# Kernel optimization log

Measured on AMD Instinct MI355X. Metric: run time of the kernel, lower is better.

## Reference

```python
import jax, jax.numpy as jnp
import numpy as np

B, S, H, NH, HD = 2, 2048, 4096, 32, 128
THETA = 10000.0


def rotate_half(x):
    x1, x2 = jnp.split(x, 2, axis=-1)
    return jnp.concatenate((-x2, x1), axis=-1)


def setup_inputs() -> dict:
    key = jax.random.key(0)
    ks = jax.random.split(key, 6)
    hidden_states = jax.random.normal(ks[0], (B, S, H), dtype=jnp.float32)
    # additive causal mask, [1,1,S,S]
    causal = jnp.triu(jnp.full((S, S), -1e9, dtype=jnp.float32), k=1)
    attention_mask = causal[None, None, :, :]
    scale = 0.02
    Wq = jax.random.normal(ks[1], (H, H), dtype=jnp.float32) * scale
    Wk = jax.random.normal(ks[2], (H, H), dtype=jnp.float32) * scale
    Wv = jax.random.normal(ks[3], (H, H), dtype=jnp.float32) * scale
    Wo = jax.random.normal(ks[4], (H, H), dtype=jnp.float32) * scale
    return {"hidden_states": hidden_states, "attention_mask": attention_mask,
            "Wq": Wq, "Wk": Wk, "Wv": Wv, "Wo": Wo}


def _rope_tables(seq_len, dtype):
    inv_freq = 1.0 / (THETA ** (jnp.arange(0, HD, 2, dtype=jnp.float32) / HD))
    t = jnp.arange(seq_len, dtype=jnp.float32)
    freqs = jnp.einsum('i,j->ij', t, inv_freq)          # [S, HD/2]
    emb = jnp.concatenate((freqs, freqs), axis=-1)       # [S, HD]
    return jnp.cos(emb).astype(dtype), jnp.sin(emb).astype(dtype)


def reference(hidden_states, attention_mask, Wq, Wk, Wv, Wo):
    b, s, _ = hidden_states.shape
    # nn.Linear: y = x @ W.T
    q = jnp.einsum('bsh,oh->bso', hidden_states, Wq).reshape(b, s, NH, HD).transpose(0, 2, 1, 3)
    k = jnp.einsum('bsh,oh->bso', hidden_states, Wk).reshape(b, s, NH, HD).transpose(0, 2, 1, 3)
    v = jnp.einsum('bsh,oh->bso', hidden_states, Wv).reshape(b, s, NH, HD).transpose(0, 2, 1, 3)
    cos, sin = _rope_tables(s, q.dtype)                  # [S, HD] broadcast over b,h
    q = q * cos + rotate_half(q) * sin
    k = k * cos + rotate_half(k) * sin
    scores = jnp.einsum('bhqd,bhkd->bhqk', q, k) / jnp.sqrt(jnp.asarray(HD, q.dtype))
    scores = scores + attention_mask
    attn = jax.nn.softmax(scores.astype(jnp.float32), axis=-1).astype(q.dtype)
    out = jnp.einsum('bhqk,bhkd->bhqd', attn, v)
    out = out.transpose(0, 2, 1, 3).reshape(b, s, H)
    return jnp.einsum('bsh,oh->bso', out, Wo)
```

## Files before the change

kernel.cpp:

```cpp
#include <hip/hip_runtime.h>
#include <stdint.h>

typedef __attribute__((ext_vector_type(4))) float f32x4;
typedef __attribute__((ext_vector_type(8))) short bf16x8;
typedef __attribute__((ext_vector_type(4))) unsigned int u32x4;

__device__ __forceinline__ short f2bf(float x) {
  unsigned int u = __builtin_bit_cast(unsigned int, x);
  unsigned int r = (u + 0x7fffu + ((u >> 16) & 1u)) >> 16;
  return (short)r;
}
__device__ __forceinline__ float bf2f(short s) {
  unsigned int u = ((unsigned int)(unsigned short)s) << 16;
  return __builtin_bit_cast(float, u);
}
__device__ __forceinline__ unsigned pkbf(float lo, float hi) {
  unsigned r;
  asm("v_cvt_pk_bf16_f32 %0, %1, %2" : "=v"(r) : "v"(lo), "v"(hi));
  return r;
}

__device__ __forceinline__ void gload_lds16(const void* g, void* l) {
  __builtin_amdgcn_global_load_lds(
      (const __attribute__((address_space(1))) void*)g,
      (__attribute__((address_space(3))) void*)l, 16, 0, 0);
}

__global__ __launch_bounds__(256) void cvt5(const float* __restrict__ a,
                                            const float* __restrict__ b,
                                            const float* __restrict__ c,
                                            const float* __restrict__ d,
                                            const float* __restrict__ e,
                                            short* __restrict__ oa,
                                            short* __restrict__ ob,
                                            short* __restrict__ oc,
                                            short* __restrict__ od,
                                            short* __restrict__ oe, int n) {
  int y = blockIdx.y;
  const float* in = (y == 0) ? a : (y == 1) ? b : (y == 2) ? c : (y == 3) ? d : e;
  short* out = (y == 0) ? oa : (y == 1) ? ob : (y == 2) ? oc : (y == 3) ? od : oe;
  int idx = blockIdx.x * blockDim.x + threadIdx.x;
  int stride = gridDim.x * blockDim.x;
  for (int i = idx * 4; i < n; i += stride * 4) {
    float4 v = *(const float4*)(in + i);
    short4 o;
    o.x = f2bf(v.x); o.y = f2bf(v.y); o.z = f2bf(v.z); o.w = f2bf(v.w);
    *(short4*)(out + i) = o;
  }
}

__global__ __launch_bounds__(256) void cvt_bf16(const float* __restrict__ in,
                                                short* __restrict__ out, int n) {
  int idx = blockIdx.x * blockDim.x + threadIdx.x;
  int stride = gridDim.x * blockDim.x;
  for (int i = idx * 4; i < n; i += stride * 4) {
    float4 v = *(const float4*)(in + i);
    short4 o;
    o.x = f2bf(v.x); o.y = f2bf(v.y); o.z = f2bf(v.z); o.w = f2bf(v.w);
    *(short4*)(out + i) = o;
  }
}

__global__ __launch_bounds__(256) void rope_table_k(float2* __restrict__ tab) {
  int idx = blockIdx.x * 256 + threadIdx.x;
  int s = idx >> 6, j = idx & 63;
  float invf = powf(10000.0f, -((float)j) / 64.0f);
  float a = (float)s * invf;
  tab[idx] = make_float2(cosf(a), sinf(a));
}

__global__ __launch_bounds__(256) void rope_apply_k(short* __restrict__ Qb,
                                                    short* __restrict__ Kb,
                                                    const float2* __restrict__ tab) {
  bool isK = (blockIdx.y != 0);
  short* base = isK ? Kb : Qb;
  float post = isK ? 1.0f : (0.08838834764831845f * 1.4426950408889634f);
  int token = blockIdx.x;
  int s = token & 2047;
  short* rowp = base + (size_t)token * 4096;
  const float2* trow = tab + s * 64;
  for (int u = threadIdx.x; u < 512; u += 256) {
    int h = u >> 4;
    int d0 = (u & 15) * 4;
    short* p1 = rowp + h * 128 + d0;
    short* p2 = p1 + 64;
    short4 a = *(short4*)p1, b = *(short4*)p2;
    short4 ra, rb;
#pragma unroll
    for (int j = 0; j < 4; ++j) {
      short aj = (&a.x)[j], bj = (&b.x)[j];
      float qa = bf2f(aj), qb = bf2f(bj);
      float2 cs = trow[d0 + j];
      (&ra.x)[j] = f2bf((qa * cs.x - qb * cs.y) * post);
      (&rb.x)[j] = f2bf((qb * cs.x + qa * cs.y) * post);
    }
    *(short4*)p1 = ra;
    *(short4*)p2 = rb;
  }
}

template <int MODE>
__global__ __launch_bounds__(512) void gemm8p(const short* __restrict__ A,
                                              const short* __restrict__ Bw,
                                              void* __restrict__ out) {
  __shared__ __attribute__((aligned(16))) short smem[2 * 32768];
  int wg = blockIdx.x;
  int xcd = wg & 7, ii = wg >> 3;
  int by = xcd * 2 + (ii >> 4);
  int bx = ii & 15;
  int tid = threadIdx.x;
  int w = tid >> 6, lane = tid & 63;
  int l16 = lane & 15, l4 = lane >> 4;
  int wm = w >> 2, wn = w & 3;

  f32x4 acc[8][4] = {};

  const short* Ab = A + (size_t)(by * 256) * 4096;
  const short* Bb = Bw + (size_t)(bx * 256) * 4096;

  auto STAGE_MAT = [&](int kt, int isB) {
    const short* src = isB ? Bb : Ab;
    int ob = (kt & 1) * 32768 + isB * 16384;
#pragma unroll
    for (int j = 0; j < 4; ++j) {
      int c = j * 512 + tid;
      int row = c >> 3;
      int sc = (c & 7) ^ (row & 7);
      gload_lds16(src + (size_t)row * 4096 + kt * 64 + sc * 8, &smem[ob + c * 8]);
    }
  };

  bf16x8 bfr[4];
  auto PHASE = [&](int ob, int kk, int mh, bool loadB) {
    const short* lA = &smem[ob];
    const short* lB = &smem[ob + 16384];
    if (loadB) {
#pragma unroll
      for (int nf = 0; nf < 4; ++nf) {
        int row = wn * 64 + nf * 16 + l16;
        int phys = (kk * 4 + l4) ^ (row & 7);
        bfr[nf] = *(const bf16x8*)&lB[row * 64 + phys * 8];
      }
    }
    bf16x8 af[4];
#pragma unroll
    for (int mf = 0; mf < 4; ++mf) {
      int row = wm * 128 + mh * 64 + mf * 16 + l16;
      int phys = (kk * 4 + l4) ^ (row & 7);
      af[mf] = *(const bf16x8*)&lA[row * 64 + phys * 8];
    }
    __builtin_amdgcn_s_setprio(1);
#pragma unroll
    for (int mf = 0; mf < 4; ++mf)
#pragma unroll
      for (int nf = 0; nf < 4; ++nf)
        acc[mh * 4 + mf][nf] =
            __builtin_amdgcn_mfma_f32_16x16x32_bf16(af[mf], bfr[nf], acc[mh * 4 + mf][nf], 0, 0, 0);
    __builtin_amdgcn_s_setprio(0);
    __builtin_amdgcn_s_barrier();
    asm volatile("" ::: "memory");
  };

  STAGE_MAT(0, 0);
  STAGE_MAT(0, 1);
  asm volatile("s_waitcnt vmcnt(0)" ::: "memory");
  __builtin_amdgcn_s_barrier();
  asm volatile("" ::: "memory");

  const int b0 = 0, b1 = 32768;
  for (int i = 0; i < 32; ++i) {
    int kt1 = 2 * i + 1;
    STAGE_MAT(kt1, 0);
    asm volatile("s_waitcnt vmcnt(4)" ::: "memory");
    __builtin_amdgcn_s_barrier();
    asm volatile("" ::: "memory");
    PHASE(b0, 0, 0, true);
    STAGE_MAT(kt1, 1);
    PHASE(b0, 0, 1, false);
    PHASE(b0, 1, 0, true);
    PHASE(b0, 1, 1, false);
    if (i + 1 < 32) {
      STAGE_MAT(2 * i + 2, 0);
      asm volatile("s_waitcnt vmcnt(4)" ::: "memory");
    } else {
      asm volatile("s_waitcnt vmcnt(0)" ::: "memory");
    }
    __builtin_amdgcn_s_barrier();
    asm volatile("" ::: "memory");
    PHASE(b1, 0, 0, true);
    if (i + 1 < 32) STAGE_MAT(2 * i + 2, 1);
    PHASE(b1, 0, 1, false);
    PHASE(b1, 1, 0, true);
    PHASE(b1, 1, 1, false);
  }

  int orow0 = by * 256 + wm * 128;
  int ocol0 = bx * 256 + wn * 64;
#pragma unroll
  for (int mf = 0; mf < 8; ++mf)
#pragma unroll
    for (int nf = 0; nf < 4; ++nf)
#pragma unroll
      for (int k = 0; k < 4; ++k) {
        int r = orow0 + mf * 16 + l4 * 4 + k;
        int c = ocol0 + nf * 16 + l16;
        float v = acc[mf][nf][k];
        if constexpr (MODE == 0) {
          ((short*)out)[(size_t)r * 4096 + c] = f2bf(v);
        } else if constexpr (MODE == 1) {
          ((float*)out)[(size_t)r * 4096 + c] = v;
        } else {
          int bb = r >> 11, ss = r & 2047;
          int h = c >> 7, d = c & 127;
          ((short*)out)[(((size_t)((bb * 32 + h) * 128 + d)) << 11) + ss] = f2bf(v);
        }
      }
}

__global__ __launch_bounds__(512, 4) void attn_k(const short* __restrict__ Qb,
                                                 const short* __restrict__ Kb,
                                                 const short* __restrict__ Vt,
                                                 short* __restrict__ AO) {
  __shared__ __attribute__((aligned(16))) short smem[24576];
  int p = blockIdx.x;
  int bh = p & 63;
  int qt = 15 - (p >> 6);
  int b = bh >> 5, h = bh & 31;
  int tid = threadIdx.x, w = tid >> 6, lane = tid & 63;
  int l16 = lane & 15, l4 = lane >> 4;

  const int nt = 2 * qt + 2;
  const int qbase = qt * 128 + w * 16;

  bf16x8 qf[4];
  {
    const short* Qg = Qb + (size_t)(b * 2048 + qbase + l16) * 4096 + h * 128 + l4 * 8;
#pragma unroll
    for (int kk = 0; kk < 4; ++kk) qf[kk] = *(const bf16x8*)(Qg + kk * 32);
  }

  f32x4 oacc[8] = {};
  float mrun = -1e30f, lsum = 0.f;

  const short* Kbase = Kb + (size_t)(b * 2048) * 4096 + h * 128;
  const short* Vbase = Vt + (size_t)bh * 128 * 2048;

  auto STAGE_K = [&](int t, int sel) {
    short* lK = &smem[sel * 8192];
#pragma unroll
    for (int j = 0; j < 2; ++j) {
      int c = j * 512 + tid;
      int row = c >> 4;
      int src = (c & 15) ^ (row & 15);
      gload_lds16(Kbase + (size_t)(t * 64 + row) * 4096 + src * 8, &lK[c * 8]);
    }
  };
  auto STAGE_V = [&](int t) {
    short* lV = &smem[16384];
#pragma unroll
    for (int j = 0; j < 2; ++j) {
      int c = j * 512 + tid;
      int row = c >> 3;
      int src = (c & 7) ^ (row & 7);
      gload_lds16(Vbase + (size_t)row * 2048 + t * 64 + src * 8, &lV[c * 8]);
    }
  };

  STAGE_V(0);
  STAGE_K(0, 0);
  STAGE_K(1, 1);

  const int src0 = l16 | ((2 * (l4 & 1)) << 4);
  const int src1 = src0 | 16;
  const bool hiA = (l4 >> 1) != 0;

  for (int t = 0; t < nt; ++t) {
    if (t == nt - 1)
      asm volatile("s_waitcnt vmcnt(0)" ::: "memory");
    else
      asm volatile("s_waitcnt vmcnt(2)" ::: "memory");
    __builtin_amdgcn_s_barrier();
    asm volatile("" ::: "memory");

    bool skip = (t * 64 > qbase + 15);
    if (!skip) {
      const short* lK = &smem[(t & 1) * 8192];
      const short* lV = &smem[16384];

      f32x4 sacc[4] = {};
#pragma unroll
      for (int kk = 0; kk < 4; ++kk) {
#pragma unroll
        for (int n4 = 0; n4 < 4; ++n4) {
          int row = n4 * 16 + l16;
          int phys = (kk * 4 + l4) ^ (row & 15);
          bf16x8 kf = *(const bf16x8*)&lK[row * 128 + phys * 8];
          sacc[n4] = __builtin_amdgcn_mfma_f32_16x16x32_bf16(kf, qf[kk], sacc[n4], 0, 0, 0);
        }
      }

      if (t * 64 + 63 > qbase) {
        int q = qbase + l16;
#pragma unroll
        for (int n4 = 0; n4 < 4; ++n4)
#pragma unroll
          for (int i = 0; i < 4; ++i) {
            int kv = t * 64 + n4 * 16 + l4 * 4 + i;
            if (kv > q) sacc[n4][i] = -1e30f;
          }
      }

      {
        float v0 = fmaxf(fmaxf(sacc[0][0], sacc[0][1]), fmaxf(sacc[0][2], sacc[0][3]));
        float v1 = fmaxf(fmaxf(sacc[1][0], sacc[1][1]), fmaxf(sacc[1][2], sacc[1][3]));
        float v2 = fmaxf(fmaxf(sacc[2][0], sacc[2][1]), fmaxf(sacc[2][2], sacc[2][3]));
        float v3 = fmaxf(fmaxf(sacc[3][0], sacc[3][1]), fmaxf(sacc[3][2], sacc[3][3]));
        float vm = fmaxf(fmaxf(v0, v1), fmaxf(v2, v3));
        vm = fmaxf(vm, __shfl_xor(vm, 16));
        vm = fmaxf(vm, __shfl_xor(vm, 32));
        if (!__all(vm - mrun <= 8.0f)) {
          float mnew = fmaxf(mrun, vm);
          float fsc = __builtin_amdgcn_exp2f(mrun - mnew);
          mrun = mnew;
          lsum *= fsc;
#pragma unroll
          for (int dg = 0; dg < 8; ++dg) oacc[dg] *= fsc;
        }
        float psum = 0.f;
#pragma unroll
        for (int n4 = 0; n4 < 4; ++n4)
#pragma unroll
          for (int i = 0; i < 4; ++i) {
            float e = __builtin_amdgcn_exp2f(sacc[n4][i] - mrun);
            sacc[n4][i] = e;
            psum += e;
          }
        psum += __shfl_xor(psum, 16);
        psum += __shfl_xor(psum, 32);
        lsum += psum;
      }

#pragma unroll
      for (int c = 0; c < 2; ++c) {
        unsigned pk0h0 = pkbf(sacc[2 * c][0], sacc[2 * c][1]);
        unsigned pk0h1 = pkbf(sacc[2 * c][2], sacc[2 * c][3]);
        unsigned pk1h0 = pkbf(sacc[2 * c + 1][0], sacc[2 * c + 1][1]);
        unsigned pk1h1 = pkbf(sacc[2 * c + 1][2], sacc[2 * c + 1][3]);
        unsigned s00 = __shfl((int)pk0h0, src0), s10 = __shfl((int)pk1h0, src0);
        unsigned s01 = __shfl((int)pk0h1, src0), s11 = __shfl((int)pk1h1, src0);
        unsigned t00 = __shfl((int)pk0h0, src1), t10 = __shfl((int)pk1h0, src1);
        unsigned t01 = __shfl((int)pk0h1, src1), t11 = __shfl((int)pk1h1, src1);
        u32x4 uw;
        uw[0] = hiA ? s10 : s00;
        uw[1] = hiA ? s11 : s01;
        uw[2] = hiA ? t10 : t00;
        uw[3] = hiA ? t11 : t01;
        bf16x8 pb = __builtin_bit_cast(bf16x8, uw);
#pragma unroll
        for (int dg = 0; dg < 8; ++dg) {
          int d = dg * 16 + l16;
          int phys = (c * 4 + l4) ^ (l16 & 7);
          bf16x8 vf = *(const bf16x8*)&lV[d * 64 + phys * 8];
          oacc[dg] = __builtin_amdgcn_mfma_f32_16x16x32_bf16(vf, pb, oacc[dg], 0, 0, 0);
        }
      }
    }

    __builtin_amdgcn_s_barrier();
    asm volatile("" ::: "memory");
    if (t + 1 < nt) STAGE_V(t + 1);
    if (t + 2 < nt) STAGE_K(t + 2, t & 1);
  }

  __syncthreads();
  short* reg = &smem[w * 2048];
  float rls = 1.0f / lsum;
#pragma unroll
  for (int dg = 0; dg < 8; ++dg) {
    unsigned u0 = pkbf(oacc[dg][0] * rls, oacc[dg][1] * rls);
    unsigned u1 = pkbf(oacc[dg][2] * rls, oacc[dg][3] * rls);
    int cc = dg * 2 + (l4 >> 1);
    int phys = cc ^ l16;
    int sidx = l16 * 128 + phys * 8 + (l4 & 1) * 4;
    *(uint2*)&reg[sidx] = make_uint2(u0, u1);
  }
#pragma unroll
  for (int pass = 0; pass < 4; ++pass) {
    int qloc = pass * 4 + l4;
    int phys = l16 ^ qloc;
    bf16x8 v = *(const bf16x8*)&reg[qloc * 128 + phys * 8];
    int tok = b * 2048 + qbase + qloc;
    *(bf16x8*)(AO + (size_t)tok * 4096 + h * 128 + l16 * 8) = v;
  }
}

extern "C" void kernel_launch(void* const* d_in, const int* in_sizes, int n_in,
                              void* d_out, int out_size, void* d_ws, size_t ws_size,
                              hipStream_t stream) {
  const float* X = (const float*)d_in[0];
  const float* Wq = (const float*)d_in[2];
  const float* Wk = (const float*)d_in[3];
  const float* Wv = (const float*)d_in[4];
  const float* Wo = (const float*)d_in[5];

  char* ws = (char*)d_ws;
  const size_t SEG = 32ull << 20;
  short* Xb  = (short*)(ws + 0 * SEG);
  short* Wqb = (short*)(ws + 1 * SEG);
  short* Wkb = (short*)(ws + 2 * SEG);
  short* Wvb = (short*)(ws + 3 * SEG);
  short* Qb  = (short*)(ws + 4 * SEG);
  short* Kb  = (short*)(ws + 5 * SEG);
  float2* tab = (float2*)(ws + 6 * SEG);

  bool bigws = ws_size >= 6 * SEG + (4ull << 20) + SEG;
  short* WobBig = (short*)(ws + 6 * SEG + (4ull << 20));

  const int NE = 4096 * 4096;
  if (bigws) {
    cvt5<<<dim3(2048, 5), 256, 0, stream>>>(X, Wq, Wk, Wv, Wo, Xb, Wqb, Wkb, Wvb, WobBig, NE);
  } else {
    cvt5<<<dim3(2048, 4), 256, 0, stream>>>(X, Wq, Wk, Wv, nullptr, Xb, Wqb, Wkb, Wvb, nullptr, NE);
  }
  rope_table_k<<<512, 256, 0, stream>>>(tab);

  gemm8p<0><<<256, 512, 0, stream>>>(Xb, Wqb, Qb);
  gemm8p<0><<<256, 512, 0, stream>>>(Xb, Wkb, Kb);
  short* Vtb = Wqb;
  gemm8p<2><<<256, 512, 0, stream>>>(Xb, Wvb, Vtb);

  rope_apply_k<<<dim3(4096, 2), 256, 0, stream>>>(Qb, Kb, tab);

  short* AO = Xb;
  attn_k<<<1024, 512, 0, stream>>>(Qb, Kb, Vtb, AO);

  short* Wob;
  if (bigws) {
    Wob = WobBig;
  } else {
    Wob = Wkb;
    cvt_bf16<<<2048, 256, 0, stream>>>(Wo, Wob, NE);
  }
  gemm8p<1><<<256, 512, 0, stream>>>(AO, Wob, (float*)d_out);
}
```

Measured before the change: 676.3 us.

## Restructure GEMM main loop to one compute block per k-tile with fewer barriers

The eight barrier-separated phases per pair of k-tiles become a single COMPUTE block per k-tile, leaving two workgroup barriers per k-tile. The global-to-LDS staging is reordered to match: the B half of tile t+1 is issued before compute, and the A half of tile t+2 is issued after the post-compute barrier, with vmcnt waits adjusted accordingly. The aim is to cut barrier stalls and let waves drift and overlap MFMA work with LDS reads more freely. In exchange, loads are interleaved with compute at coarser granularity, and B fragments stay live across a larger unrolled body, which may raise register pressure.

New measurement: 680.6 us. No clear change (+0.6%).

```diff
diff --git a/kernel.cpp b/kernel.cpp
--- a/kernel.cpp
+++ b/kernel.cpp
@@ -25,6 +25,8 @@
       (const __attribute__((address_space(1))) void*)g,
       (__attribute__((address_space(3))) void*)l, 16, 0, 0);
 }
+
+#define BARX() do { __builtin_amdgcn_s_barrier(); asm volatile("" ::: "memory"); } while (0)
 
 __global__ __launch_bounds__(256) void cvt5(const float* __restrict__ a,
                                             const float* __restrict__ b,
@@ -130,68 +132,54 @@
     }
   };
 
-  bf16x8 bfr[4];
-  auto PHASE = [&](int ob, int kk, int mh, bool loadB) {
-    const short* lA = &smem[ob];
-    const short* lB = &smem[ob + 16384];
-    if (loadB) {
+  auto COMPUTE = [&](int ob) {
+    bf16x8 af[4], bfr[4];
+#pragma unroll
+    for (int kk = 0; kk < 2; ++kk) {
 #pragma unroll
       for (int nf = 0; nf < 4; ++nf) {
         int row = wn * 64 + nf * 16 + l16;
         int phys = (kk * 4 + l4) ^ (row & 7);
-        bfr[nf] = *(const bf16x8*)&lB[row * 64 + phys * 8];
-      }
-    }
-    bf16x8 af[4];
-#pragma unroll
-    for (int mf = 0; mf < 4; ++mf) {
-      int row = wm * 128 + mh * 64 + mf * 16 + l16;
-      int phys = (kk * 4 + l4) ^ (row & 7);
-      af[mf] = *(const bf16x8*)&lA[row * 64 + phys * 8];
-    }
-    __builtin_amdgcn_s_setprio(1);
-#pragma unroll
-    for (int mf = 0; mf < 4; ++mf)
-#pragma unroll
-      for (int nf = 0; nf < 4; ++nf)
-        acc[mh * 4 + mf][nf] =
-            __builtin_amdgcn_mfma_f32_16x16x32_bf16(af[mf], bfr[nf], acc[mh * 4 + mf][nf], 0, 0, 0);
-    __builtin_amdgcn_s_setprio(0);
-    __builtin_amdgcn_s_barrier();
-    asm volatile("" ::: "memory");
+        bfr[nf] = *(const bf16x8*)&smem[ob + 16384 + row * 64 + phys * 8];
+      }
+#pragma unroll
+      for (int mh = 0; mh < 2; ++mh) {
+#pragma unroll
+        for (int mf = 0; mf < 4; ++mf) {
+          int row = wm * 128 + mh * 64 + mf * 16 + l16;
+          int phys = (kk * 4 + l4) ^ (row & 7);
+          af[mf] = *(const bf16x8*)&smem[ob + row * 64 + phys * 8];
+        }
+        __builtin_amdgcn_s_setprio(1);
+#pragma unroll
+        for (int mf = 0; mf < 4; ++mf)
+#pragma unroll
+          for (int nf = 0; nf < 4; ++nf)
+            acc[mh * 4 + mf][nf] =
+                __builtin_amdgcn_mfma_f32_16x16x32_bf16(af[mf], bfr[nf], acc[mh * 4 + mf][nf], 0, 0, 0);
+        __builtin_amdgcn_s_setprio(0);
+      }
+    }
   };
 
   STAGE_MAT(0, 0);
   STAGE_MAT(0, 1);
-  asm volatile("s_waitcnt vmcnt(0)" ::: "memory");
-  __builtin_amdgcn_s_barrier();
-  asm volatile("" ::: "memory");
-
-  const int b0 = 0, b1 = 32768;
-  for (int i = 0; i < 32; ++i) {
-    int kt1 = 2 * i + 1;
-    STAGE_MAT(kt1, 0);
-    asm volatile("s_waitcnt vmcnt(4)" ::: "memory");
-    __builtin_amdgcn_s_barrier();
-    asm volatile("" ::: "memory");
-    PHASE(b0, 0, 0, true);
-    STAGE_MAT(kt1, 1);
-    PHASE(b0, 0, 1, false);
-    PHASE(b0, 1, 0, true);
-    PHASE(b0, 1, 1, false);
-    if (i + 1 < 32) {
-      STAGE_MAT(2 * i + 2, 0);
+  STAGE_MAT(1, 0);
+  asm volatile("s_waitcnt vmcnt(4)" ::: "memory");
+  BARX();
+
+  for (int t = 0; t < 64; ++t) {
+    int ob = (t & 1) * 32768;
+    if (t + 1 < 64) STAGE_MAT(t + 1, 1);
+    COMPUTE(ob);
+    BARX();
+    if (t + 2 < 64) {
+      STAGE_MAT(t + 2, 0);
       asm volatile("s_waitcnt vmcnt(4)" ::: "memory");
-    } else {
+    } else if (t + 1 < 64) {
       asm volatile("s_waitcnt vmcnt(0)" ::: "memory");
     }
-    __builtin_amdgcn_s_barrier();
-    asm volatile("" ::: "memory");
-    PHASE(b1, 0, 0, true);
-    if (i + 1 < 32) STAGE_MAT(2 * i + 2, 1);
-    PHASE(b1, 0, 1, false);
-    PHASE(b1, 1, 0, true);
-    PHASE(b1, 1, 1, false);
+    if (t + 1 < 64) BARX();
   }
 
   int orow0 = by * 256 + wm * 128;
```
